# Performance work log

Measured on AMD Instinct MI355X. Metric: run time of the kernel, lower is better.

Reference implementation:

```python
import jax, jax.numpy as jnp
import numpy as np

N_NODES = 100000
N_EDGES = 1600000
D = 128
N_GRAPHS = 1024
N_LAYERS = 3
BN_EPS = 1e-5


def setup_inputs() -> dict:
    key = jax.random.key(0)
    ks = jax.random.split(key, 12)
    x = jax.random.normal(ks[0], (N_NODES, D), dtype=jnp.float32)
    edge_index = jax.random.randint(ks[1], (2, N_EDGES), 0, N_NODES, dtype=jnp.int32)
    batch = jnp.sort(jax.random.randint(ks[2], (N_NODES,), 0, N_GRAPHS, dtype=jnp.int32))
    scale = 1.0 / np.sqrt(D)
    W1 = jax.random.uniform(ks[3], (D, D), jnp.float32, -scale, scale)
    b1 = jax.random.uniform(ks[4], (D,), jnp.float32, -scale, scale)
    W2 = jax.random.uniform(ks[5], (D, D), jnp.float32, -scale, scale)
    b2 = jax.random.uniform(ks[6], (D,), jnp.float32, -scale, scale)
    W3 = jax.random.uniform(ks[7], (D, D), jnp.float32, -scale, scale)
    b3 = jax.random.uniform(ks[8], (D,), jnp.float32, -scale, scale)
    eps = jnp.zeros((N_LAYERS,), jnp.float32)          # GINConv train_eps init = 0
    gamma = jnp.ones((N_LAYERS, D), jnp.float32)       # BatchNorm1d weight
    beta = jnp.zeros((N_LAYERS, D), jnp.float32)       # BatchNorm1d bias
    return {"x": x, "edge_index": edge_index, "batch": batch,
            "W1": W1, "b1": b1, "W2": W2, "b2": b2, "W3": W3, "b3": b3,
            "eps": eps, "gamma": gamma, "beta": beta}


def _gin_layer(h, src, dst, W, b, eps_i, g, bt):
    # scatter-add neighbor aggregation: sum_{j in N(i)} h_j
    agg = jax.ops.segment_sum(h[src], dst, num_segments=N_NODES)  # [N, D]
    h = (1.0 + eps_i) * h + agg
    h = h @ W.T + b                                   # Linear
    mean = jnp.mean(h, axis=0)                        # BatchNorm1d (training, biased var)
    var = jnp.var(h, axis=0)
    h = (h - mean) * jax.lax.rsqrt(var + BN_EPS) * g + bt
    return jax.nn.relu(h)


def reference(x, edge_index, batch, W1, b1, W2, b2, W3, b3, eps, gamma, beta):
    src, dst = edge_index[0], edge_index[1]
    h = x
    for i, (W, b) in enumerate([(W1, b1), (W2, b2), (W3, b3)]):
        h = _gin_layer(h, src, dst, W, b, eps[i], gamma[i], beta[i])
    # global mean pool over graphs
    sums = jax.ops.segment_sum(h, batch, num_segments=N_GRAPHS)             # [G, D]
    counts = jax.ops.segment_sum(jnp.ones((h.shape[0],), h.dtype), batch,
                                 num_segments=N_GRAPHS)                      # [G]
    return sums / jnp.maximum(counts, 1.0)[:, None]
```

## Files before the change

kernel.cpp:

```cpp
#include <hip/hip_runtime.h>

#define N_NODES 100000
#define N_PAD 100032
#define N_EDGES 1600000
#define DIM 128
#define N_GRAPHS 1024

#define SCAN_BLOCK 256
#define SCAN_NB ((N_NODES + SCAN_BLOCK - 1) / SCAN_BLOCK)

#define NPART 8
#define PART_SZ 12500

typedef __bf16 bf16x8 __attribute__((ext_vector_type(8)));
typedef float f32x4 __attribute__((ext_vector_type(4)));

__device__ __forceinline__ unsigned short f2bf(float f) {
    unsigned u = __builtin_bit_cast(unsigned, f);
    u += 0x7fffu + ((u >> 16) & 1u);
    return (unsigned short)(u >> 16);
}
__device__ __forceinline__ unsigned pk2(float a, float b) {
    return (unsigned)f2bf(a) | ((unsigned)f2bf(b) << 16);
}
__device__ __forceinline__ float bf2f(unsigned short s) {
    return __builtin_bit_cast(float, (unsigned)s << 16);
}
__device__ __forceinline__ void dec2(unsigned p, float& lo, float& hi) {
    lo = __builtin_bit_cast(float, p << 16);
    hi = __builtin_bit_cast(float, p & 0xffff0000u);
}

template <bool BN>
__device__ __forceinline__ void acc8(uint4 p, float* a, const float* sc, const float* sh) {
    float v[8];
    dec2(p.x, v[0], v[1]);
    dec2(p.y, v[2], v[3]);
    dec2(p.z, v[4], v[5]);
    dec2(p.w, v[6], v[7]);
#pragma unroll
    for (int j = 0; j < 8; ++j) {
        float t = BN ? fmaxf(fmaf(v[j], sc[j], sh[j]), 0.f) : v[j];
        a[j] += t;
    }
}


__global__ __launch_bounds__(256) void hist_part_kernel(const int* __restrict__ dst,
                                                        int* __restrict__ deg) {
    int p = blockIdx.x & (NPART - 1);
    int bgrp = blockIdx.x >> 3;
    int nb = gridDim.x >> 3;
    int tid = bgrp * blockDim.x + threadIdx.x;
    int nthreads = nb * blockDim.x;
    const int NE8 = N_EDGES / 8;
    for (int i = tid; i < NE8; i += nthreads) {
        int4 a = ((const int4*)dst)[2 * i];
        int4 b = ((const int4*)dst)[2 * i + 1];
        if (a.x / PART_SZ == p) atomicAdd(&deg[a.x], 1);
        if (a.y / PART_SZ == p) atomicAdd(&deg[a.y], 1);
        if (a.z / PART_SZ == p) atomicAdd(&deg[a.z], 1);
        if (a.w / PART_SZ == p) atomicAdd(&deg[a.w], 1);
        if (b.x / PART_SZ == p) atomicAdd(&deg[b.x], 1);
        if (b.y / PART_SZ == p) atomicAdd(&deg[b.y], 1);
        if (b.z / PART_SZ == p) atomicAdd(&deg[b.z], 1);
        if (b.w / PART_SZ == p) atomicAdd(&deg[b.w], 1);
    }
}

__global__ __launch_bounds__(256) void fill_part_kernel(const int* __restrict__ src,
                                                        const int* __restrict__ dst,
                                                        int* __restrict__ cursor,
                                                        int* __restrict__ csr) {
    int p = blockIdx.x & (NPART - 1);
    int bgrp = blockIdx.x >> 3;
    int nb = gridDim.x >> 3;
    int tid = bgrp * blockDim.x + threadIdx.x;
    int nthreads = nb * blockDim.x;
    const int NE8 = N_EDGES / 8;
    for (int i = tid; i < NE8; i += nthreads) {
        int4 da = ((const int4*)dst)[2 * i];
        int4 db = ((const int4*)dst)[2 * i + 1];
        int4 sa = ((const int4*)src)[2 * i];
        int4 sb = ((const int4*)src)[2 * i + 1];
        if (da.x / PART_SZ == p) csr[atomicAdd(&cursor[da.x], 1)] = sa.x;
        if (da.y / PART_SZ == p) csr[atomicAdd(&cursor[da.y], 1)] = sa.y;
        if (da.z / PART_SZ == p) csr[atomicAdd(&cursor[da.z], 1)] = sa.z;
        if (da.w / PART_SZ == p) csr[atomicAdd(&cursor[da.w], 1)] = sa.w;
        if (db.x / PART_SZ == p) csr[atomicAdd(&cursor[db.x], 1)] = sb.x;
        if (db.y / PART_SZ == p) csr[atomicAdd(&cursor[db.y], 1)] = sb.y;
        if (db.z / PART_SZ == p) csr[atomicAdd(&cursor[db.z], 1)] = sb.z;
        if (db.w / PART_SZ == p) csr[atomicAdd(&cursor[db.w], 1)] = sb.w;
    }
}


__global__ __launch_bounds__(SCAN_BLOCK) void scan_partial_kernel(const int* __restrict__ deg,
                                                                  int* __restrict__ partials) {
    __shared__ int red[SCAN_BLOCK / 64];
    int i = blockIdx.x * SCAN_BLOCK + threadIdx.x;
    int v = (i < N_NODES) ? deg[i] : 0;
    for (int o = 32; o > 0; o >>= 1) v += __shfl_down(v, o, 64);
    if ((threadIdx.x & 63) == 0) red[threadIdx.x >> 6] = v;
    __syncthreads();
    if (threadIdx.x == 0) {
        int s = 0;
#pragma unroll
        for (int w = 0; w < SCAN_BLOCK / 64; ++w) s += red[w];
        partials[blockIdx.x] = s;
    }
}

__global__ __launch_bounds__(512) void scan_partials_kernel(int* __restrict__ partials,
                                                            int* __restrict__ off) {
    __shared__ int sm[512];
    int t = threadIdx.x;
    int v = (t < SCAN_NB) ? partials[t] : 0;
    sm[t] = v;
    __syncthreads();
    for (int o = 1; o < 512; o <<= 1) {
        int u = (t >= o) ? sm[t - o] : 0;
        __syncthreads();
        sm[t] += u;
        __syncthreads();
    }
    if (t < SCAN_NB) partials[t] = sm[t] - v;
    if (t == 0) off[N_NODES] = sm[511];
}

__global__ __launch_bounds__(SCAN_BLOCK) void scan_scatter_kernel(const int* __restrict__ deg,
                                                                  const int* __restrict__ partials,
                                                                  int* __restrict__ off,
                                                                  int* __restrict__ cursor) {
    __shared__ int sm[SCAN_BLOCK];
    int t = threadIdx.x;
    int i = blockIdx.x * SCAN_BLOCK + t;
    int v = (i < N_NODES) ? deg[i] : 0;
    sm[t] = v;
    __syncthreads();
    for (int o = 1; o < SCAN_BLOCK; o <<= 1) {
        int u = (t >= o) ? sm[t - o] : 0;
        __syncthreads();
        sm[t] += u;
        __syncthreads();
    }
    if (i < N_NODES) {
        int r = partials[blockIdx.x] + sm[t] - v;
        off[i] = r;
        cursor[i] = r;
    }
}


__global__ __launch_bounds__(64) void wprep_kernel(const float* __restrict__ W1,
                                                   const float* __restrict__ W2,
                                                   const float* __restrict__ W3,
                                                   uint4* __restrict__ wb4) {
    int b = blockIdx.x;
    int l = b >> 5;
    int nt = (b >> 2) & 7;
    int kk = b & 3;
    int lane = threadIdx.x;
    const float* W = (l == 0) ? W1 : (l == 1) ? W2 : W3;
    int row = nt * 16 + (lane & 15);
    int cb = kk * 32 + (lane >> 4) * 8;
    const float* g = W + row * DIM + cb;
    float4 f0 = *(const float4*)g;
    float4 f1 = *(const float4*)(g + 4);
    uint4 o;
    o.x = pk2(f0.x, f0.y);
    o.y = pk2(f0.z, f0.w);
    o.z = pk2(f1.x, f1.y);
    o.w = pk2(f1.z, f1.w);
    wb4[(size_t)b * 64 + lane] = o;
}


__global__ __launch_bounds__(256) void xconv_kernel(const float* __restrict__ x,
                                                    unsigned short* __restrict__ xb) {
    int i = blockIdx.x * blockDim.x + threadIdx.x;
    int stride = gridDim.x * blockDim.x;
    const int TOT = N_PAD * DIM / 8;
    for (; i < TOT; i += stride) {
        int row = i >> 4;
        int ks = i & 15;
        uint4 o = {0, 0, 0, 0};
        if (row < N_NODES) {
            const float* g = x + (size_t)row * DIM + ks * 8;
            float4 f0 = *(const float4*)g;
            float4 f1 = *(const float4*)(g + 4);
            o.x = pk2(f0.x, f0.y);
            o.y = pk2(f0.z, f0.w);
            o.z = pk2(f1.x, f1.y);
            o.w = pk2(f1.z, f1.w);
        }
        ((uint4*)xb)[i] = o;
    }
}


template <bool BN>
__global__ __launch_bounds__(256) void agg_gemm_kernel(const unsigned short* __restrict__ hin,
                                                       const int* __restrict__ off,
                                                       const int* __restrict__ csr,
                                                       const float* __restrict__ eps_arr, int layer,
                                                       const float* __restrict__ csum_prev,
                                                       const float* __restrict__ csq_prev,
                                                       const float* __restrict__ gamma_prev,
                                                       const float* __restrict__ beta_prev,
                                                       const uint4* __restrict__ wb4,
                                                       unsigned short* __restrict__ y,
                                                       float* __restrict__ csum_out,
                                                       float* __restrict__ csq_out) {
    __shared__ unsigned short tile[64 * DIM];
    __shared__ float sstat[4][DIM];
    __shared__ float sstatq[4][DIM];
    int tid = threadIdx.x;
    int row0 = blockIdx.x * 64;
    int grp = tid >> 4;
    int lane = tid & 15;
    float se = 1.0f + eps_arr[layer];
    float sc[8], sh[8];
    if (BN) {
#pragma unroll
        for (int j = 0; j < 8; ++j) {
            int d = lane * 8 + j;
            float m = csum_prev[d] * (1.0f / N_NODES);
            float var = csq_prev[d] * (1.0f / N_NODES) - m * m;
            float s = gamma_prev[d] * rsqrtf(var + 1e-5f);
            sc[j] = s;
            sh[j] = beta_prev[d] - m * s;
        }
    }
    const uint4* base = (const uint4*)hin + lane;
    const size_t RS = DIM / 8;

#pragma unroll 1
    for (int r4 = 0; r4 < 4; ++r4) {
        int trow = grp * 4 + r4;
        int row = row0 + trow;
        float a[8] = {0.f, 0.f, 0.f, 0.f, 0.f, 0.f, 0.f, 0.f};
        if (row < N_NODES) {
            {
                uint4 pv = base[(size_t)row * RS];
                float v[8];
                dec2(pv.x, v[0], v[1]); dec2(pv.y, v[2], v[3]);
                dec2(pv.z, v[4], v[5]); dec2(pv.w, v[6], v[7]);
#pragma unroll
                for (int j = 0; j < 8; ++j) {
                    float t = BN ? fmaxf(fmaf(v[j], sc[j], sh[j]), 0.f) : v[j];
                    a[j] = se * t;
                }
            }
            int k = off[row], e = off[row + 1];
            for (; k + 7 < e; k += 8) {
                int s0 = csr[k], s1 = csr[k + 1], s2 = csr[k + 2], s3 = csr[k + 3];
                int s4 = csr[k + 4], s5 = csr[k + 5], s6 = csr[k + 6], s7 = csr[k + 7];
                uint4 p0 = base[(size_t)s0 * RS];
                uint4 p1 = base[(size_t)s1 * RS];
                uint4 p2 = base[(size_t)s2 * RS];
                uint4 p3 = base[(size_t)s3 * RS];
                uint4 p4 = base[(size_t)s4 * RS];
                uint4 p5 = base[(size_t)s5 * RS];
                uint4 p6 = base[(size_t)s6 * RS];
                uint4 p7 = base[(size_t)s7 * RS];
                acc8<BN>(p0, a, sc, sh);
                acc8<BN>(p1, a, sc, sh);
                acc8<BN>(p2, a, sc, sh);
                acc8<BN>(p3, a, sc, sh);
                acc8<BN>(p4, a, sc, sh);
                acc8<BN>(p5, a, sc, sh);
                acc8<BN>(p6, a, sc, sh);
                acc8<BN>(p7, a, sc, sh);
            }
            if (k + 3 < e) {
                int s0 = csr[k], s1 = csr[k + 1], s2 = csr[k + 2], s3 = csr[k + 3];
                uint4 p0 = base[(size_t)s0 * RS];
                uint4 p1 = base[(size_t)s1 * RS];
                uint4 p2 = base[(size_t)s2 * RS];
                uint4 p3 = base[(size_t)s3 * RS];
                acc8<BN>(p0, a, sc, sh);
                acc8<BN>(p1, a, sc, sh);
                acc8<BN>(p2, a, sc, sh);
                acc8<BN>(p3, a, sc, sh);
                k += 4;
            }
            for (; k < e; ++k) {
                uint4 p0 = base[(size_t)csr[k] * RS];
                acc8<BN>(p0, a, sc, sh);
            }
        }
        uint4 pw;
        pw.x = pk2(a[0], a[1]);
        pw.y = pk2(a[2], a[3]);
        pw.z = pk2(a[4], a[5]);
        pw.w = pk2(a[6], a[7]);
        int byte = (trow * 256 + lane * 16) ^ ((trow & 7) << 4);
        *(uint4*)((char*)tile + byte) = pw;
    }
    __syncthreads();

    int w = tid >> 6;
    int l = tid & 63;
    int lr = l & 15;
    int lg = l >> 4;
    bf16x8 a[4];
#pragma unroll
    for (int kk = 0; kk < 4; ++kk) {
        int row = w * 16 + lr;
        int byte = (row * 256 + kk * 64 + lg * 16) ^ ((row & 7) << 4);
        a[kk] = __builtin_bit_cast(bf16x8, *(uint4*)((char*)tile + byte));
    }

#pragma unroll
    for (int nt = 0; nt < 8; ++nt) {
        f32x4 acc = {0.0f, 0.0f, 0.0f, 0.0f};
#pragma unroll
        for (int kk = 0; kk < 4; ++kk) {
            bf16x8 b = __builtin_bit_cast(bf16x8, wb4[(nt * 4 + kk) * 64 + l]);
            acc = __builtin_amdgcn_mfma_f32_16x16x32_bf16(a[kk], b, acc, 0, 0, 0);
        }
        int col = nt * 16 + lr;
        size_t base2 = (size_t)(row0 + w * 16 + lg * 4) * DIM + col;
        y[base2] = f2bf(acc[0]);
        y[base2 + DIM] = f2bf(acc[1]);
        y[base2 + 2 * DIM] = f2bf(acc[2]);
        y[base2 + 3 * DIM] = f2bf(acc[3]);
        float s = acc[0] + acc[1] + acc[2] + acc[3];
        float q = acc[0] * acc[0] + acc[1] * acc[1] + acc[2] * acc[2] + acc[3] * acc[3];
        s += __shfl_xor(s, 16);
        s += __shfl_xor(s, 32);
        q += __shfl_xor(q, 16);
        q += __shfl_xor(q, 32);
        if (lg == 0) {
            sstat[w][col] = s;
            sstatq[w][col] = q;
        }
    }
    __syncthreads();
    if (tid < DIM) {
        float s = sstat[0][tid] + sstat[1][tid] + sstat[2][tid] + sstat[3][tid];
        float q = sstatq[0][tid] + sstatq[1][tid] + sstatq[2][tid] + sstatq[3][tid];
        atomicAdd(&csum_out[tid], s);
        atomicAdd(&csq_out[tid], q);
    }
}


__global__ __launch_bounds__(128) void pool_kernel(const unsigned short* __restrict__ y,
                                                   const int* __restrict__ batch,
                                                   const float* __restrict__ csum,
                                                   const float* __restrict__ csq,
                                                   const float* __restrict__ gamma,
                                                   const float* __restrict__ beta,
                                                   float* __restrict__ out) {
    int gph = blockIdx.x;
    int d = threadIdx.x;
    float m = csum[d] * (1.0f / N_NODES);
    float var = csq[d] * (1.0f / N_NODES) - m * m;
    float sc = gamma[d] * rsqrtf(var + 1e-5f);
    float sh = beta[d] - m * sc;
    int lo = 0, hi = N_NODES;
    while (lo < hi) {
        int mid = (lo + hi) >> 1;
        if (batch[mid] < gph) lo = mid + 1; else hi = mid;
    }
    int start = lo;
    hi = N_NODES;
    while (lo < hi) {
        int mid = (lo + hi) >> 1;
        if (batch[mid] < gph + 1) lo = mid + 1; else hi = mid;
    }
    int end = lo;
    float s0 = 0.f, s1 = 0.f, s2 = 0.f, s3 = 0.f;
    int n = start;
    for (; n + 3 < end; n += 4) {
        float v0 = bf2f(y[(size_t)n * DIM + d]);
        float v1 = bf2f(y[(size_t)(n + 1) * DIM + d]);
        float v2 = bf2f(y[(size_t)(n + 2) * DIM + d]);
        float v3 = bf2f(y[(size_t)(n + 3) * DIM + d]);
        s0 += fmaxf(fmaf(v0, sc, sh), 0.0f);
        s1 += fmaxf(fmaf(v1, sc, sh), 0.0f);
        s2 += fmaxf(fmaf(v2, sc, sh), 0.0f);
        s3 += fmaxf(fmaf(v3, sc, sh), 0.0f);
    }
    for (; n < end; ++n) {
        float v = bf2f(y[(size_t)n * DIM + d]);
        s0 += fmaxf(fmaf(v, sc, sh), 0.0f);
    }
    float s = (s0 + s1) + (s2 + s3);
    out[gph * DIM + d] = s / fmaxf((float)(end - start), 1.0f);
}


extern "C" void kernel_launch(void* const* d_in, const int* in_sizes, int n_in,
                              void* d_out, int out_size, void* d_ws, size_t ws_size,
                              hipStream_t stream) {
    const float* x = (const float*)d_in[0];
    const int* ei = (const int*)d_in[1];
    const int* batch = (const int*)d_in[2];
    const float* Wp[3] = {(const float*)d_in[3], (const float*)d_in[5], (const float*)d_in[7]};
    const float* eps = (const float*)d_in[9];
    const float* gamma = (const float*)d_in[10];
    const float* beta = (const float*)d_in[11];
    float* out = (float*)d_out;

    char* ws = (char*)d_ws;
    size_t o = 0;
    auto alloc = [&](size_t bytes) {
        void* p = ws + o;
        o = (o + bytes + 255) & ~(size_t)255;
        return p;
    };
    int* deg = (int*)alloc(N_NODES * sizeof(int));
    int* off = (int*)alloc((N_NODES + 1) * sizeof(int));
    int* cursor = (int*)alloc(N_NODES * sizeof(int));
    int* partials = (int*)alloc(SCAN_NB * sizeof(int));
    int* csr = (int*)alloc(N_EDGES * sizeof(int));
    uint4* wb4 = (uint4*)alloc(3 * 8 * 4 * 64 * 16);
    float* csums = (float*)alloc(3 * DIM * sizeof(float));
    float* csqs = (float*)alloc(3 * DIM * sizeof(float));
    unsigned short* xb = (unsigned short*)alloc((size_t)N_PAD * DIM * 2);
    unsigned short* y0 = (unsigned short*)alloc((size_t)N_PAD * DIM * 2);
    unsigned short* y1 = (unsigned short*)alloc((size_t)N_PAD * DIM * 2);

    hipMemsetAsync(deg, 0, N_NODES * sizeof(int), stream);
    hipMemsetAsync(csums, 0, 3 * DIM * sizeof(float), stream);
    hipMemsetAsync(csqs, 0, 3 * DIM * sizeof(float), stream);

    hist_part_kernel<<<2048, 256, 0, stream>>>(ei + N_EDGES, deg);
    scan_partial_kernel<<<SCAN_NB, SCAN_BLOCK, 0, stream>>>(deg, partials);
    scan_partials_kernel<<<1, 512, 0, stream>>>(partials, off);
    scan_scatter_kernel<<<SCAN_NB, SCAN_BLOCK, 0, stream>>>(deg, partials, off, cursor);
    fill_part_kernel<<<2048, 256, 0, stream>>>(ei, ei + N_EDGES, cursor, csr);
    wprep_kernel<<<96, 64, 0, stream>>>(Wp[0], Wp[1], Wp[2], wb4);
    xconv_kernel<<<2048, 256, 0, stream>>>(x, xb);

    const int NBLK = N_PAD / 64;
    agg_gemm_kernel<false><<<NBLK, 256, 0, stream>>>(xb, off, csr, eps, 0,
                                                     nullptr, nullptr, nullptr, nullptr,
                                                     wb4, y0, csums, csqs);
    agg_gemm_kernel<true><<<NBLK, 256, 0, stream>>>(y0, off, csr, eps, 1,
                                                    csums, csqs, gamma, beta,
                                                    wb4 + 2048, y1, csums + DIM, csqs + DIM);
    agg_gemm_kernel<true><<<NBLK, 256, 0, stream>>>(y1, off, csr, eps, 2,
                                                    csums + DIM, csqs + DIM, gamma + DIM, beta + DIM,
                                                    wb4 + 4096, y0, csums + 2 * DIM, csqs + 2 * DIM);
    pool_kernel<<<N_GRAPHS, DIM, 0, stream>>>(y0, batch, csums + 2 * DIM, csqs + 2 * DIM,
                                              gamma + 2 * DIM, beta + 2 * DIM, out);
}
```

Baseline: 594.4 us.

## Split edge gathers across four lane groups per row and simplify degree histogram

Aggregation now assigns each wavefront 16 rows and spreads each row's neighbor list across the four 16-lane groups of the wave, combining the partial sums with cross-lane shuffles before packing to the shared tile. Each wave therefore gathers four neighbors per step instead of one group walking a whole row serially, which shortens the per-row dependency chain and balances uneven degrees within a wave. The cost is extra shuffle work and fewer independent loads in flight per lane (two instead of eight). Separately, the partitioned histogram, which read the destination array once per partition, is replaced by a single pass of unpartitioned global atomics, trading repeated reads for more scattered atomic contention.

```diff
diff --git a/kernel.cpp b/kernel.cpp
--- a/kernel.cpp
+++ b/kernel.cpp
@@ -46,25 +46,17 @@
 }
 
 
-__global__ __launch_bounds__(256) void hist_part_kernel(const int* __restrict__ dst,
-                                                        int* __restrict__ deg) {
-    int p = blockIdx.x & (NPART - 1);
-    int bgrp = blockIdx.x >> 3;
-    int nb = gridDim.x >> 3;
-    int tid = bgrp * blockDim.x + threadIdx.x;
-    int nthreads = nb * blockDim.x;
-    const int NE8 = N_EDGES / 8;
-    for (int i = tid; i < NE8; i += nthreads) {
-        int4 a = ((const int4*)dst)[2 * i];
-        int4 b = ((const int4*)dst)[2 * i + 1];
-        if (a.x / PART_SZ == p) atomicAdd(&deg[a.x], 1);
-        if (a.y / PART_SZ == p) atomicAdd(&deg[a.y], 1);
-        if (a.z / PART_SZ == p) atomicAdd(&deg[a.z], 1);
-        if (a.w / PART_SZ == p) atomicAdd(&deg[a.w], 1);
-        if (b.x / PART_SZ == p) atomicAdd(&deg[b.x], 1);
-        if (b.y / PART_SZ == p) atomicAdd(&deg[b.y], 1);
-        if (b.z / PART_SZ == p) atomicAdd(&deg[b.z], 1);
-        if (b.w / PART_SZ == p) atomicAdd(&deg[b.w], 1);
+__global__ __launch_bounds__(256) void hist_kernel(const int* __restrict__ dst,
+                                                   int* __restrict__ deg) {
+    int i = blockIdx.x * blockDim.x + threadIdx.x;
+    int stride = gridDim.x * blockDim.x;
+    const int NE4 = N_EDGES / 4;
+    for (; i < NE4; i += stride) {
+        int4 d4 = ((const int4*)dst)[i];
+        atomicAdd(&deg[d4.x], 1);
+        atomicAdd(&deg[d4.y], 1);
+        atomicAdd(&deg[d4.z], 1);
+        atomicAdd(&deg[d4.w], 1);
     }
 }
 
@@ -217,14 +209,15 @@
     __shared__ float sstatq[4][DIM];
     int tid = threadIdx.x;
     int row0 = blockIdx.x * 64;
-    int grp = tid >> 4;
-    int lane = tid & 15;
+    int wv = tid >> 6;
+    int esl = (tid >> 4) & 3;
+    int dl = tid & 15;
     float se = 1.0f + eps_arr[layer];
     float sc[8], sh[8];
     if (BN) {
 #pragma unroll
         for (int j = 0; j < 8; ++j) {
-            int d = lane * 8 + j;
+            int d = dl * 8 + j;
             float m = csum_prev[d] * (1.0f / N_NODES);
             float var = csq_prev[d] * (1.0f / N_NODES) - m * m;
             float s = gamma_prev[d] * rsqrtf(var + 1e-5f);
@@ -232,14 +225,15 @@
             sh[j] = beta_prev[d] - m * s;
         }
     }
-    const uint4* base = (const uint4*)hin + lane;
+    const uint4* base = (const uint4*)hin + dl;
     const size_t RS = DIM / 8;
 
 #pragma unroll 1
-    for (int r4 = 0; r4 < 4; ++r4) {
-        int trow = grp * 4 + r4;
+    for (int r = 0; r < 16; ++r) {
+        int trow = wv * 16 + r;
         int row = row0 + trow;
         float a[8] = {0.f, 0.f, 0.f, 0.f, 0.f, 0.f, 0.f, 0.f};
+        float s8[8] = {0.f, 0.f, 0.f, 0.f, 0.f, 0.f, 0.f, 0.f};
         if (row < N_NODES) {
             {
                 uint4 pv = base[(size_t)row * RS];
@@ -247,56 +241,41 @@
                 dec2(pv.x, v[0], v[1]); dec2(pv.y, v[2], v[3]);
                 dec2(pv.z, v[4], v[5]); dec2(pv.w, v[6], v[7]);
 #pragma unroll
-                for (int j = 0; j < 8; ++j) {
-                    float t = BN ? fmaxf(fmaf(v[j], sc[j], sh[j]), 0.f) : v[j];
-                    a[j] = se * t;
+                for (int j = 0; j < 8; ++j)
+                    s8[j] = BN ? fmaxf(fmaf(v[j], sc[j], sh[j]), 0.f) : v[j];
+            }
+            int k = off[row], e = off[row + 1];
+            for (; k + 8 <= e; k += 8) {
+                int i0 = csr[k + esl];
+                int i1 = csr[k + 4 + esl];
+                uint4 p0 = base[(size_t)i0 * RS];
+                uint4 p1 = base[(size_t)i1 * RS];
+                acc8<BN>(p0, a, sc, sh);
+                acc8<BN>(p1, a, sc, sh);
+            }
+            for (; k < e; k += 4) {
+                int kk = k + esl;
+                if (kk < e) {
+                    uint4 p0 = base[(size_t)csr[kk] * RS];
+                    acc8<BN>(p0, a, sc, sh);
                 }
             }
-            int k = off[row], e = off[row + 1];
-            for (; k + 7 < e; k += 8) {
-                int s0 = csr[k], s1 = csr[k + 1], s2 = csr[k + 2], s3 = csr[k + 3];
-                int s4 = csr[k + 4], s5 = csr[k + 5], s6 = csr[k + 6], s7 = csr[k + 7];
-                uint4 p0 = base[(size_t)s0 * RS];
-                uint4 p1 = base[(size_t)s1 * RS];
-                uint4 p2 = base[(size_t)s2 * RS];
-                uint4 p3 = base[(size_t)s3 * RS];
-                uint4 p4 = base[(size_t)s4 * RS];
-                uint4 p5 = base[(size_t)s5 * RS];
-                uint4 p6 = base[(size_t)s6 * RS];
-                uint4 p7 = base[(size_t)s7 * RS];
-                acc8<BN>(p0, a, sc, sh);
-                acc8<BN>(p1, a, sc, sh);
-                acc8<BN>(p2, a, sc, sh);
-                acc8<BN>(p3, a, sc, sh);
-                acc8<BN>(p4, a, sc, sh);
-                acc8<BN>(p5, a, sc, sh);
-                acc8<BN>(p6, a, sc, sh);
-                acc8<BN>(p7, a, sc, sh);
-            }
-            if (k + 3 < e) {
-                int s0 = csr[k], s1 = csr[k + 1], s2 = csr[k + 2], s3 = csr[k + 3];
-                uint4 p0 = base[(size_t)s0 * RS];
-                uint4 p1 = base[(size_t)s1 * RS];
-                uint4 p2 = base[(size_t)s2 * RS];
-                uint4 p3 = base[(size_t)s3 * RS];
-                acc8<BN>(p0, a, sc, sh);
-                acc8<BN>(p1, a, sc, sh);
-                acc8<BN>(p2, a, sc, sh);
-                acc8<BN>(p3, a, sc, sh);
-                k += 4;
-            }
-            for (; k < e; ++k) {
-                uint4 p0 = base[(size_t)csr[k] * RS];
-                acc8<BN>(p0, a, sc, sh);
-            }
-        }
-        uint4 pw;
-        pw.x = pk2(a[0], a[1]);
-        pw.y = pk2(a[2], a[3]);
-        pw.z = pk2(a[4], a[5]);
-        pw.w = pk2(a[6], a[7]);
-        int byte = (trow * 256 + lane * 16) ^ ((trow & 7) << 4);
-        *(uint4*)((char*)tile + byte) = pw;
+        }
+#pragma unroll
+        for (int j = 0; j < 8; ++j) {
+            a[j] += __shfl_xor(a[j], 16);
+            a[j] += __shfl_xor(a[j], 32);
+            a[j] = fmaf(se, s8[j], a[j]);
+        }
+        if (esl == 0) {
+            uint4 pw;
+            pw.x = pk2(a[0], a[1]);
+            pw.y = pk2(a[2], a[3]);
+            pw.z = pk2(a[4], a[5]);
+            pw.w = pk2(a[6], a[7]);
+            int byte = (trow * 256 + dl * 16) ^ ((trow & 7) << 4);
+            *(uint4*)((char*)tile + byte) = pw;
+        }
     }
     __syncthreads();
 
@@ -428,7 +407,7 @@
     hipMemsetAsync(csums, 0, 3 * DIM * sizeof(float), stream);
     hipMemsetAsync(csqs, 0, 3 * DIM * sizeof(float), stream);
 
-    hist_part_kernel<<<2048, 256, 0, stream>>>(ei + N_EDGES, deg);
+    hist_kernel<<<1024, 256, 0, stream>>>(ei + N_EDGES, deg);
     scan_partial_kernel<<<SCAN_NB, SCAN_BLOCK, 0, stream>>>(deg, partials);
     scan_partials_kernel<<<1, 512, 0, stream>>>(partials, off);
     scan_scatter_kernel<<<SCAN_NB, SCAN_BLOCK, 0, stream>>>(deg, partials, off, cursor);
```

New measurement: 581.5 us. 2.2% less time.
